# Optimization experiments

Measured on AMD Instinct MI355X. Metric: run time of the kernel, lower is better.

Reference implementation:

```python
import jax, jax.numpy as jnp
import numpy as np
import math

N_HEADS = 16


def setup_inputs() -> dict:
    key = jax.random.key(0)
    ks = jax.random.split(key, 5)
    B, S, E = 2, 2048, 1024
    scale = 1.0 / math.sqrt(E)
    return {
        "x": jax.random.normal(ks[0], (B, S, E), dtype=jnp.float32),
        "w_in": jax.random.normal(ks[1], (3 * E, E), dtype=jnp.float32) * scale,
        "b_in": jax.random.normal(ks[2], (3 * E,), dtype=jnp.float32) * 0.01,
        "w_out": jax.random.normal(ks[3], (E, E), dtype=jnp.float32) * scale,
        "b_out": jax.random.normal(ks[4], (E,), dtype=jnp.float32) * 0.01,
    }


def reference(x, w_in, b_in, w_out, b_out):
    B, S, E = x.shape
    H = N_HEADS
    d = E // H
    # fused QKV projection: [B,S,3E]
    qkv = x @ w_in.T + b_in
    q, k, v = jnp.split(qkv, 3, axis=-1)
    # [B,S,E] -> [B,H,S,d]
    q = q.reshape(B, S, H, d).transpose(0, 2, 1, 3)
    k = k.reshape(B, S, H, d).transpose(0, 2, 1, 3)
    v = v.reshape(B, S, H, d).transpose(0, 2, 1, 3)
    # scores [B,H,S,S], scaled by 1/sqrt(d_head) (no causal mask: casual_mask=False)
    scores = jnp.einsum("bhqd,bhkd->bhqk", q, k) / jnp.sqrt(jnp.float32(d)).astype(x.dtype)
    w = jax.nn.softmax(scores, axis=-1)
    # attention output [B,H,S,d] -> [B,S,E]
    out = jnp.einsum("bhqk,bhkd->bhqd", w, v)
    out = out.transpose(0, 2, 1, 3).reshape(B, S, E)
    return out @ w_out.T + b_out
```

## Files before the change

kernel.cpp:

```cpp
#include <hip/hip_runtime.h>
#include <cstdint>


typedef __bf16 bf16x8 __attribute__((ext_vector_type(8)));
typedef short s16x4 __attribute__((ext_vector_type(4)));
typedef float f32x4 __attribute__((ext_vector_type(4)));

__device__ __forceinline__ unsigned short f32_to_bf16_rne(float f) {
    unsigned int u = __builtin_bit_cast(unsigned int, f);
    u += 0x7FFF + ((u >> 16) & 1);
    return (unsigned short)(u >> 16);
}

__device__ __forceinline__ unsigned int pack_bf16_trunc(float a, float b) {
    unsigned int ua = __builtin_bit_cast(unsigned int, a);
    unsigned int ub = __builtin_bit_cast(unsigned int, b);
    return __builtin_amdgcn_perm(ub, ua, 0x07060302u);
}

__device__ __forceinline__ void gload16(const void* g, void* l) {
    __builtin_amdgcn_global_load_lds(
        (const __attribute__((address_space(1))) unsigned int*)g,
        (__attribute__((address_space(3))) unsigned int*)l, 16, 0, 0);
}

__global__ void cvt_all(const float* __restrict__ x, const float* __restrict__ wi,
                        const float* __restrict__ wo, unsigned short* __restrict__ xb,
                        unsigned short* __restrict__ wib, unsigned short* __restrict__ wob) {
    int i = blockIdx.x * blockDim.x + threadIdx.x;
    const float* src; unsigned short* dst; int off;
    if (i < 1048576)            { src = x;  dst = xb;  off = i; }
    else if (i < 1048576 + 786432) { src = wi; dst = wib; off = i - 1048576; }
    else                        { src = wo; dst = wob; off = i - (1048576 + 786432); }
    float4 v = ((const float4*)src)[off];
    ushort4 o;
    o.x = f32_to_bf16_rne(v.x); o.y = f32_to_bf16_rne(v.y);
    o.z = f32_to_bf16_rne(v.z); o.w = f32_to_bf16_rne(v.w);
    ((ushort4*)dst)[off] = o;
}

__launch_bounds__(256)
__global__ void gemm_qkv(const unsigned short* __restrict__ X,
                         const unsigned short* __restrict__ W,
                         const float* __restrict__ bias,
                         unsigned short* __restrict__ Qp,
                         unsigned short* __restrict__ Kp,
                         unsigned short* __restrict__ Vt) {
    __shared__ __align__(16) unsigned short As[128 * 32];
    __shared__ __align__(16) unsigned short Bs[128 * 32];
    const int t = threadIdx.x;
    const int w = t >> 6, lane = t & 63, quad = lane >> 4, l16 = lane & 15;
    const int wm = (w >> 1) * 64, wn = (w & 1) * 64;
    const int m0 = blockIdx.y * 128, n0 = blockIdx.x * 128;

    f32x4 acc[4][4] = {};

    for (int kt = 0; kt < 1024; kt += 32) {
        __syncthreads();
#pragma unroll
        for (int i = 0; i < 2; ++i) {
            int c = t + 256 * i;
            int r = c >> 2, cc = (c & 3) * 8;
            gload16(&X[(m0 + r) * 1024 + kt + cc], &As[c * 8]);
            gload16(&W[(n0 + r) * 1024 + kt + cc], &Bs[c * 8]);
        }
        __syncthreads();
        bf16x8 af[4], bw[4];
#pragma unroll
        for (int mi = 0; mi < 4; ++mi)
            af[mi] = *(const bf16x8*)&As[(wm + mi * 16 + l16) * 32 + quad * 8];
#pragma unroll
        for (int ni = 0; ni < 4; ++ni)
            bw[ni] = *(const bf16x8*)&Bs[(wn + ni * 16 + l16) * 32 + quad * 8];
#pragma unroll
        for (int mi = 0; mi < 4; ++mi)
#pragma unroll
            for (int ni = 0; ni < 4; ++ni)
                acc[mi][ni] = __builtin_amdgcn_mfma_f32_16x16x32_bf16(af[mi], bw[ni], acc[mi][ni], 0, 0, 0);
    }

    const float QSCALE = 0.125f * 1.44269504089f;
#pragma unroll
    for (int mi = 0; mi < 4; ++mi) {
#pragma unroll
        for (int ni = 0; ni < 4; ++ni) {
            int col = n0 + wn + ni * 16 + l16;
            float bv = bias[col];
            int which = col >> 10;
            int hc = col & 1023;
            int h = hc >> 6, d = hc & 63;
            int row0 = m0 + wm + mi * 16 + quad * 4;
            int b = row0 >> 11, s0 = row0 & 2047;
            int bh = b * 16 + h;
            if (which == 2) {
                ushort4 pk;
                pk.x = f32_to_bf16_rne(acc[mi][ni][0] + bv);
                pk.y = f32_to_bf16_rne(acc[mi][ni][1] + bv);
                pk.z = f32_to_bf16_rne(acc[mi][ni][2] + bv);
                pk.w = f32_to_bf16_rne(acc[mi][ni][3] + bv);
                *(ushort4*)&Vt[(bh * 64 + d) * 2048 + s0] = pk;
            } else if (which == 0) {
#pragma unroll
                for (int r = 0; r < 4; ++r)
                    Qp[(bh * 2048 + s0 + r) * 64 + d] =
                        f32_to_bf16_rne((acc[mi][ni][r] + bv) * QSCALE);
            } else {
#pragma unroll
                for (int r = 0; r < 4; ++r)
                    Kp[(bh * 2048 + s0 + r) * 64 + d] = f32_to_bf16_rne(acc[mi][ni][r] + bv);
            }
        }
    }
}

#define LDP 72
__launch_bounds__(128, 2)
__global__ void attn(const unsigned short* __restrict__ Qp, const unsigned short* __restrict__ Kp,
                     const unsigned short* __restrict__ Vt, unsigned short* __restrict__ A2) {
    __shared__ __align__(16) unsigned short Ks[2][64 * LDP];
    __shared__ __align__(16) unsigned short Vs[2][64 * LDP];
    const int t = threadIdx.x, w = t >> 6, lane = t & 63, quad = lane >> 4, l16 = lane & 15;
    const int bh = blockIdx.x;
    const int qb = blockIdx.y;
    const unsigned short* Qh = Qp + bh * (2048 * 64);
    const unsigned short* Kh = Kp + bh * (2048 * 64);
    const unsigned short* Vh = Vt + bh * (64 * 2048);

    bf16x8 qf[2][2];
#pragma unroll
    for (int nq = 0; nq < 2; ++nq)
#pragma unroll
        for (int ks = 0; ks < 2; ++ks) {
            int row = qb * 64 + w * 32 + nq * 16 + l16;
            qf[nq][ks] = *(const bf16x8*)&Qh[row * 64 + ks * 32 + quad * 8];
        }

    f32x4 o_acc[4][2] = {};
    float l_lane[2] = {0.f, 0.f};

#pragma unroll
    for (int i = 0; i < 4; ++i) {
        int c = t + 128 * i;
        int r = c >> 3, cc = (c & 7) * 8;
        *(uint4*)&Ks[0][r * LDP + cc] = *(const uint4*)&Kh[r * 64 + cc];
        *(uint4*)&Vs[0][r * LDP + cc] = *(const uint4*)&Vh[r * 2048 + cc];
    }

    int cur = 0;
    for (int it = 0; it < 32; ++it) {
        __syncthreads();
        uint4 kn[4], vn[4];
        const bool pfetch = (it != 31);
        if (pfetch) {
            int ktn = (it + 1) * 64;
#pragma unroll
            for (int i = 0; i < 4; ++i) {
                int c = t + 128 * i;
                int r = c >> 3, cc = (c & 7) * 8;
                kn[i] = *(const uint4*)&Kh[(ktn + r) * 64 + cc];
                vn[i] = *(const uint4*)&Vh[r * 2048 + ktn + cc];
            }
        }
        const unsigned short* Kc = Ks[cur];
        const unsigned short* Vc = Vs[cur];

        f32x4 s_acc[4][2] = {};
#pragma unroll
        for (int ks = 0; ks < 2; ++ks)
#pragma unroll
            for (int mi = 0; mi < 4; ++mi) {
                bf16x8 kf = *(const bf16x8*)&Kc[(mi * 16 + l16) * LDP + ks * 32 + quad * 8];
#pragma unroll
                for (int nq = 0; nq < 2; ++nq)
                    s_acc[mi][nq] = __builtin_amdgcn_mfma_f32_16x16x32_bf16(kf, qf[nq][ks], s_acc[mi][nq], 0, 0, 0);
            }

        s16x4 bq[4][2];
#pragma unroll
        for (int nq = 0; nq < 2; ++nq) {
            float rsum = 0.f;
#pragma unroll
            for (int mi = 0; mi < 4; ++mi) {
                float p0 = exp2f(s_acc[mi][nq][0]);
                float p1 = exp2f(s_acc[mi][nq][1]);
                float p2 = exp2f(s_acc[mi][nq][2]);
                float p3 = exp2f(s_acc[mi][nq][3]);
                rsum += (p0 + p1) + (p2 + p3);
                uint2 pk;
                pk.x = pack_bf16_trunc(p0, p1);
                pk.y = pack_bf16_trunc(p2, p3);
                bq[mi][nq] = __builtin_bit_cast(s16x4, pk);
            }
            l_lane[nq] += rsum;
        }

#pragma unroll
        for (int dm = 0; dm < 4; ++dm)
#pragma unroll
            for (int kt4 = 0; kt4 < 4; ++kt4) {
                s16x4 av = __builtin_bit_cast(s16x4,
                    *(const uint2*)&Vc[(dm * 16 + l16) * LDP + kt4 * 16 + quad * 4]);
#pragma unroll
                for (int nq = 0; nq < 2; ++nq)
                    o_acc[dm][nq] = __builtin_amdgcn_mfma_f32_16x16x16bf16_1k(av, bq[kt4][nq], o_acc[dm][nq], 0, 0, 0);
            }

        if (pfetch) {
#pragma unroll
            for (int i = 0; i < 4; ++i) {
                int c = t + 128 * i;
                int r = c >> 3, cc = (c & 7) * 8;
                *(uint4*)&Ks[cur ^ 1][r * LDP + cc] = kn[i];
                *(uint4*)&Vs[cur ^ 1][r * LDP + cc] = vn[i];
            }
        }
        cur ^= 1;
    }

    const int b = bh >> 4, h = bh & 15;
#pragma unroll
    for (int nq = 0; nq < 2; ++nq) {
        float l = l_lane[nq];
        l += __shfl_xor(l, 16);
        l += __shfl_xor(l, 32);
        float rl = 1.0f / l;
        int s = qb * 64 + w * 32 + nq * 16 + l16;
        int tok = b * 2048 + s;
#pragma unroll
        for (int dm = 0; dm < 4; ++dm) {
            ushort4 o;
            o.x = f32_to_bf16_rne(o_acc[dm][nq][0] * rl);
            o.y = f32_to_bf16_rne(o_acc[dm][nq][1] * rl);
            o.z = f32_to_bf16_rne(o_acc[dm][nq][2] * rl);
            o.w = f32_to_bf16_rne(o_acc[dm][nq][3] * rl);
            *(ushort4*)&A2[tok * 1024 + h * 64 + dm * 16 + quad * 4] = o;
        }
    }
}

__launch_bounds__(256)
__global__ void gemm_out_k(const unsigned short* __restrict__ A, const unsigned short* __restrict__ W,
                           const float* __restrict__ bias, float* __restrict__ out) {
    __shared__ __align__(16) unsigned short As[128 * 32];
    __shared__ __align__(16) unsigned short Bs[64 * 32];
    const int t = threadIdx.x;
    const int w = t >> 6, lane = t & 63, quad = lane >> 4, l16 = lane & 15;
    const int wm = (w >> 1) * 64, wn = (w & 1) * 32;
    const int m0 = blockIdx.y * 128, n0 = blockIdx.x * 64;

    f32x4 acc[4][2] = {};

    for (int kt = 0; kt < 1024; kt += 32) {
        __syncthreads();
#pragma unroll
        for (int i = 0; i < 2; ++i) {
            int c = t + 256 * i;
            int r = c >> 2, cc = (c & 3) * 8;
            gload16(&A[(m0 + r) * 1024 + kt + cc], &As[c * 8]);
        }
        {
            int c = t;
            int r = c >> 2, cc = (c & 3) * 8;
            gload16(&W[(n0 + r) * 1024 + kt + cc], &Bs[c * 8]);
        }
        __syncthreads();
        bf16x8 af[4], bw[2];
#pragma unroll
        for (int mi = 0; mi < 4; ++mi)
            af[mi] = *(const bf16x8*)&As[(wm + mi * 16 + l16) * 32 + quad * 8];
#pragma unroll
        for (int ni = 0; ni < 2; ++ni)
            bw[ni] = *(const bf16x8*)&Bs[(wn + ni * 16 + l16) * 32 + quad * 8];
#pragma unroll
        for (int mi = 0; mi < 4; ++mi)
#pragma unroll
            for (int ni = 0; ni < 2; ++ni)
                acc[mi][ni] = __builtin_amdgcn_mfma_f32_16x16x32_bf16(af[mi], bw[ni], acc[mi][ni], 0, 0, 0);
    }

#pragma unroll
    for (int mi = 0; mi < 4; ++mi)
#pragma unroll
        for (int ni = 0; ni < 2; ++ni) {
            int col = n0 + wn + ni * 16 + l16;
            float bv = bias[col];
#pragma unroll
            for (int r = 0; r < 4; ++r) {
                int row = m0 + wm + mi * 16 + quad * 4 + r;
                out[row * 1024 + col] = acc[mi][ni][r] + bv;
            }
        }
}

extern "C" void kernel_launch(void* const* d_in, const int* in_sizes, int n_in,
                              void* d_out, int out_size, void* d_ws, size_t ws_size,
                              hipStream_t stream) {
    const float* x     = (const float*)d_in[0];
    const float* w_in  = (const float*)d_in[1];
    const float* b_in  = (const float*)d_in[2];
    const float* w_out = (const float*)d_in[3];
    const float* b_out = (const float*)d_in[4];
    float* out = (float*)d_out;

    char* ws = (char*)d_ws;
    unsigned short* xb  = (unsigned short*)(ws);
    unsigned short* wib = (unsigned short*)(ws + 8388608);
    unsigned short* wob = (unsigned short*)(ws + 14680064);
    unsigned short* Qp  = (unsigned short*)(ws + 16777216);
    unsigned short* Kp  = (unsigned short*)(ws + 25165824);
    unsigned short* Vt  = (unsigned short*)(ws + 33554432);
    unsigned short* A2  = (unsigned short*)(ws + 41943040);

    cvt_all<<<8192, 256, 0, stream>>>(x, w_in, w_out, xb, wib, wob);
    gemm_qkv<<<dim3(24, 32), 256, 0, stream>>>(xb, wib, b_in, Qp, Kp, Vt);
    attn<<<dim3(32, 32), 128, 0, stream>>>(Qp, Kp, Vt, A2);
    gemm_out_k<<<dim3(16, 32), 256, 0, stream>>>(A2, wob, b_out, out);
}
```

Baseline: 215.5 us.

## Split attention over key halves and merge partial results in a combine kernel

The attention kernel now splits the key range in two, so each block handles 128 queries over half the keys. K and V tiles are read straight from global memory into registers rather than staged through double-buffered LDS. Unnormalized fp32 partial outputs and row sums go to workspace, and a new combine kernel adds the halves, normalizes, and writes bf16. This targets LDS traffic and barriers and raises parallelism. In exchange it adds fp32 partial-output writes and reads, an extra launch, and redundant global K/V loads across waves, which lean on cache hits.

```diff
diff --git a/kernel.cpp b/kernel.cpp
--- a/kernel.cpp
+++ b/kernel.cpp
@@ -113,67 +113,56 @@
     }
 }
 
-#define LDP 72
-__launch_bounds__(128, 2)
-__global__ void attn(const unsigned short* __restrict__ Qp, const unsigned short* __restrict__ Kp,
-                     const unsigned short* __restrict__ Vt, unsigned short* __restrict__ A2) {
-    __shared__ __align__(16) unsigned short Ks[2][64 * LDP];
-    __shared__ __align__(16) unsigned short Vs[2][64 * LDP];
+__launch_bounds__(256, 3)
+__global__ void attn_ks(const unsigned short* __restrict__ Qp, const unsigned short* __restrict__ Kp,
+                        const unsigned short* __restrict__ Vt,
+                        float* __restrict__ Po, float* __restrict__ Pl) {
     const int t = threadIdx.x, w = t >> 6, lane = t & 63, quad = lane >> 4, l16 = lane & 15;
-    const int bh = blockIdx.x;
-    const int qb = blockIdx.y;
+    const int bh = blockIdx.x & 31;
+    const int rest = blockIdx.x >> 5;
+    const int split = rest & 1;
+    const int qg = rest >> 1;
+    const int q0 = (qg * 4 + w) * 32;
     const unsigned short* Qh = Qp + bh * (2048 * 64);
     const unsigned short* Kh = Kp + bh * (2048 * 64);
     const unsigned short* Vh = Vt + bh * (64 * 2048);
+    const int k0 = split * 1024;
 
     bf16x8 qf[2][2];
 #pragma unroll
     for (int nq = 0; nq < 2; ++nq)
 #pragma unroll
-        for (int ks = 0; ks < 2; ++ks) {
-            int row = qb * 64 + w * 32 + nq * 16 + l16;
-            qf[nq][ks] = *(const bf16x8*)&Qh[row * 64 + ks * 32 + quad * 8];
-        }
+        for (int ks = 0; ks < 2; ++ks)
+            qf[nq][ks] = *(const bf16x8*)&Qh[(q0 + nq * 16 + l16) * 64 + ks * 32 + quad * 8];
 
     f32x4 o_acc[4][2] = {};
     float l_lane[2] = {0.f, 0.f};
 
-#pragma unroll
-    for (int i = 0; i < 4; ++i) {
-        int c = t + 128 * i;
-        int r = c >> 3, cc = (c & 7) * 8;
-        *(uint4*)&Ks[0][r * LDP + cc] = *(const uint4*)&Kh[r * 64 + cc];
-        *(uint4*)&Vs[0][r * LDP + cc] = *(const uint4*)&Vh[r * 2048 + cc];
-    }
-
-    int cur = 0;
-    for (int it = 0; it < 32; ++it) {
-        __syncthreads();
-        uint4 kn[4], vn[4];
-        const bool pfetch = (it != 31);
-        if (pfetch) {
-            int ktn = (it + 1) * 64;
-#pragma unroll
-            for (int i = 0; i < 4; ++i) {
-                int c = t + 128 * i;
-                int r = c >> 3, cc = (c & 7) * 8;
-                kn[i] = *(const uint4*)&Kh[(ktn + r) * 64 + cc];
-                vn[i] = *(const uint4*)&Vh[r * 2048 + ktn + cc];
-            }
-        }
-        const unsigned short* Kc = Ks[cur];
-        const unsigned short* Vc = Vs[cur];
+    for (int it = 0; it < 16; ++it) {
+        const int kt = k0 + it * 64;
+
+        bf16x8 kf[2][4];
+#pragma unroll
+        for (int ks = 0; ks < 2; ++ks)
+#pragma unroll
+            for (int mi = 0; mi < 4; ++mi)
+                kf[ks][mi] = *(const bf16x8*)&Kh[(kt + mi * 16 + l16) * 64 + ks * 32 + quad * 8];
 
         f32x4 s_acc[4][2] = {};
 #pragma unroll
         for (int ks = 0; ks < 2; ++ks)
 #pragma unroll
-            for (int mi = 0; mi < 4; ++mi) {
-                bf16x8 kf = *(const bf16x8*)&Kc[(mi * 16 + l16) * LDP + ks * 32 + quad * 8];
+            for (int mi = 0; mi < 4; ++mi)
 #pragma unroll
                 for (int nq = 0; nq < 2; ++nq)
-                    s_acc[mi][nq] = __builtin_amdgcn_mfma_f32_16x16x32_bf16(kf, qf[nq][ks], s_acc[mi][nq], 0, 0, 0);
-            }
+                    s_acc[mi][nq] = __builtin_amdgcn_mfma_f32_16x16x32_bf16(kf[ks][mi], qf[nq][ks], s_acc[mi][nq], 0, 0, 0);
+
+        uint2 av[4][4];
+#pragma unroll
+        for (int dm = 0; dm < 4; ++dm)
+#pragma unroll
+            for (int kt4 = 0; kt4 < 4; ++kt4)
+                av[dm][kt4] = *(const uint2*)&Vh[(dm * 16 + l16) * 2048 + kt + kt4 * 16 + quad * 4];
 
         s16x4 bq[4][2];
 #pragma unroll
@@ -198,44 +187,49 @@
         for (int dm = 0; dm < 4; ++dm)
 #pragma unroll
             for (int kt4 = 0; kt4 < 4; ++kt4) {
-                s16x4 av = __builtin_bit_cast(s16x4,
-                    *(const uint2*)&Vc[(dm * 16 + l16) * LDP + kt4 * 16 + quad * 4]);
+                s16x4 avv = __builtin_bit_cast(s16x4, av[dm][kt4]);
 #pragma unroll
                 for (int nq = 0; nq < 2; ++nq)
-                    o_acc[dm][nq] = __builtin_amdgcn_mfma_f32_16x16x16bf16_1k(av, bq[kt4][nq], o_acc[dm][nq], 0, 0, 0);
+                    o_acc[dm][nq] = __builtin_amdgcn_mfma_f32_16x16x16bf16_1k(avv, bq[kt4][nq], o_acc[dm][nq], 0, 0, 0);
             }
-
-        if (pfetch) {
-#pragma unroll
-            for (int i = 0; i < 4; ++i) {
-                int c = t + 128 * i;
-                int r = c >> 3, cc = (c & 7) * 8;
-                *(uint4*)&Ks[cur ^ 1][r * LDP + cc] = kn[i];
-                *(uint4*)&Vs[cur ^ 1][r * LDP + cc] = vn[i];
-            }
-        }
-        cur ^= 1;
-    }
-
-    const int b = bh >> 4, h = bh & 15;
+    }
+
 #pragma unroll
     for (int nq = 0; nq < 2; ++nq) {
         float l = l_lane[nq];
         l += __shfl_xor(l, 16);
         l += __shfl_xor(l, 32);
-        float rl = 1.0f / l;
-        int s = qb * 64 + w * 32 + nq * 16 + l16;
-        int tok = b * 2048 + s;
-#pragma unroll
-        for (int dm = 0; dm < 4; ++dm) {
-            ushort4 o;
-            o.x = f32_to_bf16_rne(o_acc[dm][nq][0] * rl);
-            o.y = f32_to_bf16_rne(o_acc[dm][nq][1] * rl);
-            o.z = f32_to_bf16_rne(o_acc[dm][nq][2] * rl);
-            o.w = f32_to_bf16_rne(o_acc[dm][nq][3] * rl);
-            *(ushort4*)&A2[tok * 1024 + h * 64 + dm * 16 + quad * 4] = o;
-        }
-    }
+        int q = q0 + nq * 16 + l16;
+        size_t base = ((size_t)(split * 32 + bh) * 2048 + q) * 64;
+#pragma unroll
+        for (int dm = 0; dm < 4; ++dm)
+            *(float4*)&Po[base + dm * 16 + quad * 4] = __builtin_bit_cast(float4, o_acc[dm][nq]);
+        if (quad == 0)
+            Pl[(split * 32 + bh) * 2048 + q] = l;
+    }
+}
+
+__global__ void attn_combine(const float* __restrict__ Po, const float* __restrict__ Pl,
+                             unsigned short* __restrict__ A2) {
+    int i = blockIdx.x * blockDim.x + threadIdx.x;
+    int bh = i >> 15;
+    int rem = i & 32767;
+    int q = rem >> 4;
+    int d = (rem & 15) * 4;
+    size_t base = ((size_t)bh * 2048 + q) * 64 + d;
+    const size_t SPLIT = (size_t)32 * 2048 * 64;
+    float4 o0 = *(const float4*)&Po[base];
+    float4 o1 = *(const float4*)&Po[base + SPLIT];
+    float l = Pl[bh * 2048 + q] + Pl[32 * 2048 + bh * 2048 + q];
+    float rl = 1.0f / l;
+    int tok = (bh >> 4) * 2048 + q;
+    int col = (bh & 15) * 64 + d;
+    ushort4 o;
+    o.x = f32_to_bf16_rne((o0.x + o1.x) * rl);
+    o.y = f32_to_bf16_rne((o0.y + o1.y) * rl);
+    o.z = f32_to_bf16_rne((o0.z + o1.z) * rl);
+    o.w = f32_to_bf16_rne((o0.w + o1.w) * rl);
+    *(ushort4*)&A2[(size_t)tok * 1024 + col] = o;
 }
 
 __launch_bounds__(256)
@@ -310,9 +304,12 @@
     unsigned short* Kp  = (unsigned short*)(ws + 25165824);
     unsigned short* Vt  = (unsigned short*)(ws + 33554432);
     unsigned short* A2  = (unsigned short*)(ws + 41943040);
+    float*          Po  = (float*)(ws + 50331648);
+    float*          Pl  = (float*)(ws + 50331648 + 33554432);
 
     cvt_all<<<8192, 256, 0, stream>>>(x, w_in, w_out, xb, wib, wob);
     gemm_qkv<<<dim3(24, 32), 256, 0, stream>>>(xb, wib, b_in, Qp, Kp, Vt);
-    attn<<<dim3(32, 32), 128, 0, stream>>>(Qp, Kp, Vt, A2);
+    attn_ks<<<1024, 256, 0, stream>>>(Qp, Kp, Vt, Po, Pl);
+    attn_combine<<<4096, 256, 0, stream>>>(Po, Pl, A2);
     gemm_out_k<<<dim3(16, 32), 256, 0, stream>>>(A2, wob, b_out, out);
 }
```

Result: slower. 339.6 us (+57.6%).
